# Kernel tuning notes

Measured on AMD Instinct MI355X. Metric: run time of the kernel, lower is better.

The kernel has to match this reference:

```python
import jax, jax.numpy as jnp
import numpy as np
import math


def setup_inputs() -> dict:
    key = jax.random.key(0)
    ks = jax.random.split(key, 8)
    B, S, dim = 4, 1024, 2048
    H, D = 16, 128          # n_heads = dim // core_dim
    T = 1024                # cached kv length
    w_scale = 1.0 / math.sqrt(dim)
    return {
        "x": jax.random.normal(ks[0], (B, S, dim), dtype=jnp.float32),
        "k_cache": jax.random.normal(ks[1], (B, H, T, D), dtype=jnp.float32),
        "v_cache": jax.random.normal(ks[2], (B, H, T, D), dtype=jnp.float32),
        "Wq": jax.random.normal(ks[3], (dim, dim), dtype=jnp.float32) * w_scale,
        "bq": jnp.zeros((dim,), jnp.float32),
        "Wk": jax.random.normal(ks[4], (dim, dim), dtype=jnp.float32) * w_scale,
        "bk": jnp.zeros((dim,), jnp.float32),
        "Wv": jax.random.normal(ks[5], (dim, dim), dtype=jnp.float32) * w_scale,
        "bv": jnp.zeros((dim,), jnp.float32),
        "Wo": jax.random.normal(ks[6], (dim, dim), dtype=jnp.float32) * w_scale,
        "bo": jnp.zeros((dim,), jnp.float32),
    }


def _split_heads(t, H):
    # [B, S, dim] -> [B, H, S, D]
    B, S, dim = t.shape
    return t.reshape(B, S, H, dim // H).transpose(0, 2, 1, 3)


def reference(x, k_cache, v_cache, Wq, bq, Wk, bk, Wv, bv, Wo, bo):
    B, S, dim = x.shape
    H = k_cache.shape[1]
    D = dim // H
    T = k_cache.shape[2]

    q = _split_heads(x @ Wq.T + bq, H)                 # [B,H,S,D]
    k_new = _split_heads(x @ Wk.T + bk, H)             # [B,H,S,D]
    v_new = _split_heads(x @ Wv.T + bv, H)

    k = jnp.concatenate([k_cache, k_new], axis=2)      # [B,H,T+S,D]
    v = jnp.concatenate([v_cache, v_new], axis=2)

    scale = 1.0 / math.sqrt(D)
    scores = jnp.einsum("bhqd,bhkd->bhqk", q, k) * scale   # [B,H,S,T+S]

    # causal mask with cache offset: query i may attend to key j iff j <= i + T
    q_pos = jnp.arange(S)[:, None] + T
    k_pos = jnp.arange(T + S)[None, :]
    mask = k_pos <= q_pos                              # [S, T+S]
    scores = jnp.where(mask[None, None], scores, jnp.finfo(scores.dtype).min)

    attn = jax.nn.softmax(scores, axis=-1)
    ctx = jnp.einsum("bhqk,bhkd->bhqd", attn, v)       # [B,H,S,D]
    ctx = ctx.transpose(0, 2, 1, 3).reshape(B, S, dim) # merge heads

    out = ctx @ Wo.T + bo                              # dropout is identity (p=0 / eval)
    return (out, k, v)
```

## Files before the change

kernel.cpp:

```cpp
#include <hip/hip_runtime.h>
#include <hip/hip_bf16.h>

typedef float f32x4 __attribute__((ext_vector_type(4)));
typedef __bf16 bf16x8 __attribute__((ext_vector_type(8)));
typedef unsigned short u16x8 __attribute__((ext_vector_type(8)));

#define DIMK 2048
#define QSCALE ((float)(0.08838834764831845 * 1.4426950408889634))

__device__ __forceinline__ unsigned short f2bf(float f) {
    union { float f; unsigned int u; } v; v.f = f;
    unsigned int r = v.u + 0x7fffu + ((v.u >> 16) & 1u);
    return (unsigned short)(r >> 16);
}
__device__ __forceinline__ float bf2f(unsigned short u) {
    union { unsigned int i; float f; } v; v.i = ((unsigned int)u) << 16; return v.f;
}

__device__ __forceinline__ void lds_load16(void* lds, const void* gsrc) {
    __builtin_amdgcn_global_load_lds(
        (const __attribute__((address_space(1))) unsigned int*)gsrc,
        (__attribute__((address_space(3))) unsigned int*)lds,
        16, 0, 0);
}

__device__ __forceinline__ int vperm4(int kv4) {
    return ((kv4 >> 5) << 5) + (((kv4 >> 2) & 3) << 3) + (((kv4 >> 4) & 1) << 2);
}

__global__ __launch_bounds__(256) void prep_all(
    const float* __restrict__ x,  const float* __restrict__ Wq,
    const float* __restrict__ Wk, const float* __restrict__ Wv,
    const float* __restrict__ Wo,
    const float* __restrict__ kc, const float* __restrict__ vc,
    unsigned short* __restrict__ xbf, unsigned short* __restrict__ Wqb,
    unsigned short* __restrict__ Wkb, unsigned short* __restrict__ Wvb,
    unsigned short* __restrict__ Wob,
    float* __restrict__ kout, unsigned short* __restrict__ Kbf,
    float* __restrict__ vout, unsigned short* __restrict__ Vtp)
{
    const int bid = blockIdx.x;
    const int tid = threadIdx.x;

    if (bid < 24576) {
        int i = bid * 256 + tid;
        const float* src; unsigned short* dst; size_t off;
        if (i < 2097152) { src = x; dst = xbf; off = i; }
        else {
            int j = (i - 2097152) >> 20;
            off = (size_t)((i - 2097152) & 1048575);
            src = j == 0 ? Wq : j == 1 ? Wk : j == 2 ? Wv : Wo;
            dst = j == 0 ? Wqb : j == 1 ? Wkb : j == 2 ? Wvb : Wob;
        }
        f32x4 v = *(const f32x4*)(src + off * 4);
        ushort4 pk = { f2bf(v[0]), f2bf(v[1]), f2bf(v[2]), f2bf(v[3]) };
        *(ushort4*)(dst + off * 4) = pk;
    } else if (bid < 32768) {
        size_t i4 = (size_t)(bid - 24576) * 256 + tid;
        size_t e = i4 * 4;
        size_t bh = e >> 17, rem = e & 131071;
        f32x4 v = *(const f32x4*)(kc + e);
        size_t dsto = (bh << 18) + rem;
        *(f32x4*)(kout + dsto) = v;
        ushort4 pk = { f2bf(v[0]), f2bf(v[1]), f2bf(v[2]), f2bf(v[3]) };
        *(ushort4*)(Kbf + dsto) = pk;
    } else {
        __shared__ unsigned short T[128 * 72];
        const int o = bid - 32768;
        const int t = o & 15;
        const int kv0 = t * 64;
        const int bh = o >> 4;
        const float* src = vc + ((size_t)bh << 17) + (size_t)kv0 * 128;
        float* vdst = vout + ((size_t)bh << 18) + (size_t)kv0 * 128;
        #pragma unroll
        for (int r = 0; r < 8; ++r) {
            int e4 = r * 256 + tid;
            int kv = e4 >> 5, d0 = (e4 & 31) << 2;
            f32x4 v = *(const f32x4*)(src + kv * 128 + d0);
            *(f32x4*)(vdst + kv * 128 + d0) = v;
            #pragma unroll
            for (int i = 0; i < 4; ++i) T[(d0 + i) * 72 + kv] = f2bf(v[i]);
        }
        __syncthreads();
        unsigned short* tile = Vtp + ((size_t)bh * 32 + t) * 8192;
        #pragma unroll
        for (int r = 0; r < 8; ++r) {
            int e = r * 256 + tid;
            int d = e >> 4, k4 = (e & 15) << 2;
            ushort4 pk = { T[d * 72 + k4], T[d * 72 + k4 + 1], T[d * 72 + k4 + 2], T[d * 72 + k4 + 3] };
            const int idx = d * 64 + (vperm4(k4) ^ ((d & 7) << 3));
            *(ushort4*)(tile + idx) = pk;
        }
    }
}

__device__ __forceinline__ void gemm_core64(
    const unsigned short* __restrict__ A16, const unsigned short* __restrict__ W16,
    int m0, int n0, int tid, int w, int g, int c, int wr, int wc,
    unsigned short* As, unsigned short* Bs, f32x4 (&acc)[4][4])
{
    const int srow = tid >> 3;
    const int schk = (tid & 7) ^ (srow & 7);
    const unsigned short* Asrc = A16 + (size_t)(m0 + srow) * DIMK + schk * 8;
    const unsigned short* Bsrc = W16 + (size_t)(n0 + srow) * DIMK + schk * 8;
    const int cswz = (c & 7) << 3;

    for (int k0 = 0; k0 < DIMK; k0 += 64) {
        __syncthreads();
        #pragma unroll
        for (int r = 0; r < 4; ++r) {
            lds_load16(As + r * 2048 + w * 512, Asrc + (size_t)r * 32 * DIMK + k0);
            lds_load16(Bs + r * 2048 + w * 512, Bsrc + (size_t)r * 32 * DIMK + k0);
        }
        __syncthreads();

        #pragma unroll
        for (int kd = 0; kd < 2; ++kd) {
            const int ko = (kd * 32 + g * 8) ^ cswz;
            bf16x8 af[4], bfr[4];
            #pragma unroll
            for (int i = 0; i < 4; ++i)
                af[i] = *(const bf16x8*)(&As[(wr * 64 + i * 16 + c) * 64 + ko]);
            #pragma unroll
            for (int i = 0; i < 4; ++i)
                bfr[i] = *(const bf16x8*)(&Bs[(wc * 64 + i * 16 + c) * 64 + ko]);
            #pragma unroll
            for (int i = 0; i < 4; ++i)
                #pragma unroll
                for (int j = 0; j < 4; ++j)
                    acc[i][j] = __builtin_amdgcn_mfma_f32_16x16x32_bf16(af[i], bfr[j], acc[i][j], 0, 0, 0);
        }
    }
}

__global__ __launch_bounds__(256) void gemm_qkv(
    const unsigned short* __restrict__ xbf,
    const unsigned short* __restrict__ Wqb, const unsigned short* __restrict__ Wkb,
    const unsigned short* __restrict__ Wvb,
    const float* __restrict__ bq, const float* __restrict__ bk, const float* __restrict__ bv,
    unsigned short* __restrict__ Qbf,
    float* __restrict__ kout, unsigned short* __restrict__ Kbf,
    float* __restrict__ vout, unsigned short* __restrict__ Vtp)
{
    const int o = blockIdx.x;
    const int xcd = o & 7;
    const int k = o >> 3;
    const int mblk = k & 31;
    const int nloc = k >> 5;
    const int nblk = xcd * 6 + nloc;
    const int m0 = mblk * 128;
    const int n0g = nblk * 128;
    const int mi = n0g >> 11;
    const int n0 = n0g & 2047;

    const unsigned short* W16 = mi == 0 ? Wqb : (mi == 1 ? Wkb : Wvb);
    const float* bias = mi == 0 ? bq : (mi == 1 ? bk : bv);

    const int tid = threadIdx.x;
    const int lane = tid & 63;
    const int w = tid >> 6;
    const int g = lane >> 4;
    const int c = lane & 15;
    const int wr = w >> 1, wc = w & 1;

    __shared__ unsigned short As[128 * 64];
    __shared__ unsigned short Bs[128 * 64];

    f32x4 acc[4][4];
    #pragma unroll
    for (int i = 0; i < 4; ++i)
        #pragma unroll
        for (int j = 0; j < 4; ++j)
            acc[i][j] = f32x4{0.f, 0.f, 0.f, 0.f};

    gemm_core64(xbf, W16, m0, n0, tid, w, g, c, wr, wc, As, Bs, acc);

    #pragma unroll
    for (int j = 0; j < 4; ++j) {
        const int n = n0 + wc * 64 + j * 16 + c;
        const float bn = bias[n];
        const int hh = n >> 7, d = n & 127;
        #pragma unroll
        for (int i = 0; i < 4; ++i) {
            float y4[4];
            #pragma unroll
            for (int tq = 0; tq < 4; ++tq) y4[tq] = acc[i][j][tq] + bn;
            const int mb = m0 + wr * 64 + i * 16 + g * 4;
            if (mi == 0) {
                #pragma unroll
                for (int tq = 0; tq < 4; ++tq) {
                    int m = mb + tq; int b = m >> 10, s = m & 1023;
                    Qbf[((((size_t)b * 16 + hh) << 10) + s) * 128 + d] = f2bf(y4[tq] * QSCALE);
                }
            } else if (mi == 1) {
                #pragma unroll
                for (int tq = 0; tq < 4; ++tq) {
                    int m = mb + tq; int b = m >> 10, s = m & 1023;
                    kout[(((size_t)b * 16 + hh) * 2048 + 1024 + s) * 128 + d] = y4[tq];
                    Kbf[(((size_t)b * 16 + hh) << 18) + (size_t)(1024 + s) * 128 + d] = f2bf(y4[tq]);
                }
            } else {
                #pragma unroll
                for (int tq = 0; tq < 4; ++tq) {
                    int m = mb + tq; int b = m >> 10, s = m & 1023;
                    vout[(((size_t)b * 16 + hh) * 2048 + 1024 + s) * 128 + d] = y4[tq];
                }
                int b = mb >> 10, s = mb & 1023;
                const int t = 16 + (s >> 6);
                const int idx = d * 64 + (vperm4(s & 63) ^ ((d & 7) << 3));
                ushort4 pk = { f2bf(y4[0]), f2bf(y4[1]), f2bf(y4[2]), f2bf(y4[3]) };
                *(ushort4*)(Vtp + ((size_t)(b * 16 + hh) * 32 + t) * 8192 + idx) = pk;
            }
        }
    }
}

__global__ __launch_bounds__(256) void gemm_wo(
    const unsigned short* __restrict__ ctx, const unsigned short* __restrict__ Wob,
    const float* __restrict__ bo, float* __restrict__ outp)
{
    const int o = blockIdx.x;
    const int xcd = o & 7;
    const int k = o >> 3;
    const int mblk = k & 31;
    const int nloc = k >> 5;
    const int nblk = xcd * 2 + nloc;
    const int m0 = mblk * 128;
    const int n0 = nblk * 128;

    const int tid = threadIdx.x;
    const int lane = tid & 63;
    const int w = tid >> 6;
    const int g = lane >> 4;
    const int c = lane & 15;
    const int wr = w >> 1, wc = w & 1;

    __shared__ unsigned short As[128 * 64];
    __shared__ unsigned short Bs[128 * 64];

    f32x4 acc[4][4];
    #pragma unroll
    for (int i = 0; i < 4; ++i)
        #pragma unroll
        for (int j = 0; j < 4; ++j)
            acc[i][j] = f32x4{0.f, 0.f, 0.f, 0.f};

    gemm_core64(ctx, Wob, m0, n0, tid, w, g, c, wr, wc, As, Bs, acc);

    #pragma unroll
    for (int j = 0; j < 4; ++j) {
        const int n = n0 + wc * 64 + j * 16 + c;
        const float bn = bo[n];
        #pragma unroll
        for (int i = 0; i < 4; ++i) {
            const int mb = m0 + wr * 64 + i * 16 + g * 4;
            #pragma unroll
            for (int tq = 0; tq < 4; ++tq)
                outp[(size_t)(mb + tq) * 2048 + n] = acc[i][j][tq] + bn;
        }
    }
}

__global__ __launch_bounds__(512) void attn9(
    const unsigned short* __restrict__ Qbf,
    const unsigned short* __restrict__ Kbf,
    const unsigned short* __restrict__ Vtp,
    unsigned short* __restrict__ Pp,
    float* __restrict__ Mp,
    float* __restrict__ Lp)
{
    const int o = blockIdx.x;
    const int xcd = o & 7;
    const int kk0 = o >> 3;
    const int half = kk0 & 1;
    const int qt = 7 - ((kk0 >> 1) & 7);
    const int bh = (kk0 >> 4) * 8 + xcd;

    const int tid = threadIdx.x;
    const int lane = tid & 63;
    const int w = tid >> 6;
    const int g = lane >> 4;
    const int c = lane & 15;
    const int cswz = (c & 7) << 3;

    __shared__ unsigned short Ks[2][64 * 128];
    __shared__ unsigned short Vs[2][64 * 128];

    const unsigned short* Qb = Qbf + ((size_t)bh * 1024 + qt * 128) * 128;
    const unsigned short* Kb = Kbf + ((size_t)bh << 18);
    const unsigned short* Vtile = Vtp + (size_t)bh * 32 * 8192;

    bf16x8 aq[4];
    #pragma unroll
    for (int kd = 0; kd < 4; ++kd)
        aq[kd] = *(const bf16x8*)(Qb + (w * 16 + c) * 128 + kd * 32 + g * 8);

    f32x4 od[8];
    #pragma unroll
    for (int nf = 0; nf < 8; ++nf)
        od[nf] = f32x4{0.f, 0.f, 0.f, 0.f};
    float mrow = -1e30f, lrow = 0.f;

    const int krow = tid >> 4;
    const int kswz = (((tid & 15) << 4) ^ ((krow & 7) << 4)) >> 1;
    const unsigned short* Kl = Kb + (size_t)krow * 128 + kswz;

    const int cnt = 9 + qt;
    const int t0 = half * cnt;
    const int limw = 1024 + qt * 128 + w * 16;

    {
        const int kv0 = t0 * 64;
        lds_load16(&Ks[0][w * 512], Kl + (size_t)kv0 * 128);
        lds_load16(&Ks[0][4096 + w * 512], Kl + (size_t)(kv0 + 32) * 128);
        const unsigned short* Vsrc = Vtile + (size_t)t0 * 8192 + tid * 8;
        lds_load16(&Vs[0][w * 512], Vsrc);
        lds_load16(&Vs[0][4096 + w * 512], Vsrc + 4096);
        __syncthreads();
    }

    int cur = 0;
    for (int t = t0; t < t0 + cnt; ++t) {
        const int kv0 = t * 64;
        const bool next = (t + 1 < t0 + cnt);

        if (next) {
            const int kvn = kv0 + 64;
            lds_load16(&Ks[cur ^ 1][w * 512], Kl + (size_t)kvn * 128);
            lds_load16(&Ks[cur ^ 1][4096 + w * 512], Kl + (size_t)(kvn + 32) * 128);
            const unsigned short* Vsrc = Vtile + (size_t)(t + 1) * 8192 + tid * 8;
            lds_load16(&Vs[cur ^ 1][w * 512], Vsrc);
            lds_load16(&Vs[cur ^ 1][4096 + w * 512], Vsrc + 4096);
        }

        const unsigned short* Ksc = &Ks[cur][0];
        const unsigned short* Vsc = &Vs[cur][0];

        f32x4 sc[4];
        #pragma unroll
        for (int n = 0; n < 4; ++n)
            sc[n] = f32x4{0.f, 0.f, 0.f, 0.f};
        #pragma unroll
        for (int kd = 0; kd < 4; ++kd) {
            bf16x8 bk[4];
            #pragma unroll
            for (int n = 0; n < 4; ++n)
                bk[n] = *(const bf16x8*)(&Ksc[(n * 16 + c) * 128 + ((kd * 32 + g * 8) ^ cswz)]);
            #pragma unroll
            for (int n = 0; n < 4; ++n)
                sc[n] = __builtin_amdgcn_mfma_f32_16x16x32_bf16(bk[n], aq[kd], sc[n], 0, 0, 0);
        }

        const bool need_mask = (kv0 + 63 > limw);
        if (need_mask) {
            const int lim = limw + c;
            #pragma unroll
            for (int n = 0; n < 4; ++n)
                #pragma unroll
                for (int j = 0; j < 4; ++j)
                    if (kv0 + n * 16 + g * 4 + j > lim) sc[n][j] = -1e30f;
        }
        {
            float t4[4];
            #pragma unroll
            for (int n = 0; n < 4; ++n)
                t4[n] = fmaxf(fmaxf(sc[n][0], sc[n][1]), fmaxf(sc[n][2], sc[n][3]));
            float rmax = fmaxf(fmaxf(t4[0], t4[1]), fmaxf(t4[2], t4[3]));
            rmax = fmaxf(rmax, __shfl_xor(rmax, 16));
            rmax = fmaxf(rmax, __shfl_xor(rmax, 32));

            if (!__all(rmax <= mrow + 8.0f)) {
                const float mnew = fmaxf(mrow, rmax);
                const float fs = exp2f(mrow - mnew);
                mrow = mnew;
                lrow *= fs;
                #pragma unroll
                for (int j = 0; j < 4; ++j) {
                    const float fsj = __shfl(fs, (lane & 48) | (g * 4 + j));
                    #pragma unroll
                    for (int nf = 0; nf < 8; ++nf)
                        od[nf][j] *= fsj;
                }
            }
            const float mm = mrow;
            float s4[4];
            #pragma unroll
            for (int n = 0; n < 4; ++n) {
                #pragma unroll
                for (int j = 0; j < 4; ++j)
                    sc[n][j] = exp2f(sc[n][j] - mm);
                s4[n] = (sc[n][0] + sc[n][1]) + (sc[n][2] + sc[n][3]);
            }
            float rsum = (s4[0] + s4[1]) + (s4[2] + s4[3]);
            rsum += __shfl_xor(rsum, 16);
            rsum += __shfl_xor(rsum, 32);
            lrow += rsum;
        }

        bf16x8 pa[2];
        #pragma unroll
        for (int kk = 0; kk < 2; ++kk)
            #pragma unroll
            for (int e = 0; e < 8; ++e)
                pa[kk][e] = (__bf16)sc[2 * kk + (e >> 2)][e & 3];

        #pragma unroll
        for (int kk = 0; kk < 2; ++kk) {
            #pragma unroll
            for (int nf = 0; nf < 8; ++nf) {
                bf16x8 bv = *(const bf16x8*)(&Vsc[(nf * 16 + c) * 64 + ((kk * 32 + g * 8) ^ cswz)]);
                od[nf] = __builtin_amdgcn_mfma_f32_16x16x32_bf16(pa[kk], bv, od[nf], 0, 0, 0);
            }
        }

        __syncthreads();
        cur ^= 1;
    }

    const size_t pbase = ((size_t)(half * 64 + bh) * 1024 + qt * 128) * 128;
    const int mlbase = (half * 64 + bh) * 1024 + qt * 128;
    if (lane < 16) {
        Mp[mlbase + w * 16 + c] = mrow;
        Lp[mlbase + w * 16 + c] = lrow;
    }
    #pragma unroll
    for (int j = 0; j < 4; ++j) {
        const float lj = __shfl(lrow, (lane & 48) | (g * 4 + j));
        const float rl = 1.0f / lj;
        const int ql = w * 16 + g * 4 + j;
        #pragma unroll
        for (int nf = 0; nf < 8; ++nf)
            Pp[pbase + (size_t)ql * 128 + nf * 16 + c] = f2bf(od[nf][j] * rl);
    }
}

__global__ __launch_bounds__(256) void merge_ctx(
    const unsigned short* __restrict__ Pp, const float* __restrict__ Mp,
    const float* __restrict__ Lp, unsigned short* __restrict__ ctx)
{
    const int idx = blockIdx.x * 256 + threadIdx.x;
    const int r = idx >> 4;
    const int dc = (idx & 15) << 3;
    const float m0 = Mp[r], m1 = Mp[65536 + r];
    const float l0 = Lp[r], l1 = Lp[65536 + r];
    const float M = fmaxf(m0, m1);
    float w0 = l0 * exp2f(m0 - M);
    float w1 = l1 * exp2f(m1 - M);
    const float inv = 1.0f / (w0 + w1);
    w0 *= inv; w1 *= inv;
    u16x8 a = *(const u16x8*)(Pp + (size_t)r * 128 + dc);
    u16x8 bb = *(const u16x8*)(Pp + (size_t)8388608 + (size_t)r * 128 + dc);
    const int bh = r >> 10, q = r & 1023;
    unsigned short* dst = ctx + ((size_t)(bh >> 4) * 1024 + q) * 2048 + (bh & 15) * 128 + dc;
    u16x8 outv;
    #pragma unroll
    for (int e = 0; e < 8; ++e)
        outv[e] = f2bf(w0 * bf2f(a[e]) + w1 * bf2f(bb[e]));
    *(u16x8*)dst = outv;
}

__global__ __launch_bounds__(256) void copy_cache(
    const float* __restrict__ kc, const float* __restrict__ vc,
    float* __restrict__ kout, float* __restrict__ vout)
{
    size_t i4 = (size_t)blockIdx.x * 256 + threadIdx.x;
    const float* src = blockIdx.y ? vc : kc;
    float* dst = blockIdx.y ? vout : kout;
    size_t e = i4 * 4;
    size_t bh = e >> 17, rem = e & 131071;
    f32x4 v = *(const f32x4*)(src + e);
    *(f32x4*)(dst + (bh << 18) + rem) = v;
}

template<int MODE, bool ABF16>
__global__ __launch_bounds__(256) void gemm_bt(
    const void* __restrict__ Ag, const float* __restrict__ Wf,
    const float* __restrict__ bias, void* __restrict__ dst)
{
    const int tid = threadIdx.x;
    const int lane = tid & 63;
    const int w = tid >> 6;
    const int g = lane >> 4;
    const int c = lane & 15;
    const int wr = w >> 1, wc = w & 1;
    const int m0 = blockIdx.y * 128;
    const int n0 = blockIdx.x * 128;

    __shared__ unsigned short As[128 * 40];
    __shared__ unsigned short Bs[128 * 40];

    f32x4 acc[4][4];
    #pragma unroll
    for (int i = 0; i < 4; ++i)
        #pragma unroll
        for (int j = 0; j < 4; ++j)
            acc[i][j] = f32x4{0.f, 0.f, 0.f, 0.f};

    for (int k0 = 0; k0 < DIMK; k0 += 32) {
        __syncthreads();
        if constexpr (ABF16) {
            const unsigned short* A16 = (const unsigned short*)Ag;
            #pragma unroll
            for (int r = 0; r < 2; ++r) {
                int e8 = r * 256 + tid;
                int row = e8 >> 2, col = (e8 & 3) << 3;
                *(uint4*)(&As[row * 40 + col]) =
                    *(const uint4*)(A16 + (size_t)(m0 + row) * DIMK + k0 + col);
            }
        } else {
            const float* Af = (const float*)Ag;
            #pragma unroll
            for (int r = 0; r < 4; ++r) {
                int e4 = r * 256 + tid;
                int row = e4 >> 3, col = (e4 & 7) << 2;
                f32x4 v = *(const f32x4*)(Af + (size_t)(m0 + row) * DIMK + k0 + col);
                ushort4 pk = { f2bf(v[0]), f2bf(v[1]), f2bf(v[2]), f2bf(v[3]) };
                *(ushort4*)(&As[row * 40 + col]) = pk;
            }
        }
        {
            #pragma unroll
            for (int r = 0; r < 4; ++r) {
                int e4 = r * 256 + tid;
                int row = e4 >> 3, col = (e4 & 7) << 2;
                f32x4 v = *(const f32x4*)(Wf + (size_t)(n0 + row) * DIMK + k0 + col);
                ushort4 pk = { f2bf(v[0]), f2bf(v[1]), f2bf(v[2]), f2bf(v[3]) };
                *(ushort4*)(&Bs[row * 40 + col]) = pk;
            }
        }
        __syncthreads();

        bf16x8 af[4], bfr[4];
        #pragma unroll
        for (int i = 0; i < 4; ++i)
            af[i] = *(const bf16x8*)(&As[(wr * 64 + i * 16 + c) * 40 + g * 8]);
        #pragma unroll
        for (int i = 0; i < 4; ++i)
            bfr[i] = *(const bf16x8*)(&Bs[(wc * 64 + i * 16 + c) * 40 + g * 8]);
        #pragma unroll
        for (int i = 0; i < 4; ++i)
            #pragma unroll
            for (int j = 0; j < 4; ++j)
                acc[i][j] = __builtin_amdgcn_mfma_f32_16x16x32_bf16(af[i], bfr[j], acc[i][j], 0, 0, 0);
    }

    #pragma unroll
    for (int j = 0; j < 4; ++j) {
        const int n = n0 + wc * 64 + j * 16 + c;
        const float bn = bias[n];
        #pragma unroll
        for (int i = 0; i < 4; ++i) {
            float y4[4];
            #pragma unroll
            for (int tq = 0; tq < 4; ++tq) y4[tq] = acc[i][j][tq] + bn;
            const int mb = m0 + wr * 64 + i * 16 + g * 4;
            if constexpr (MODE == 0) {
                #pragma unroll
                for (int tq = 0; tq < 4; ++tq) {
                    int m = mb + tq; int b = m >> 10, s = m & 1023;
                    int hh = n >> 7, d = n & 127;
                    ((unsigned short*)dst)[((((size_t)b * 16 + hh) << 10) + s) * 128 + d] = f2bf(y4[tq] * QSCALE);
                }
            } else if constexpr (MODE == 1) {
                #pragma unroll
                for (int tq = 0; tq < 4; ++tq) {
                    int m = mb + tq; int b = m >> 10, s = m & 1023;
                    int hh = n >> 7, d = n & 127;
                    ((float*)dst)[(((size_t)b * 16 + hh) * 2048 + 1024 + s) * 128 + d] = y4[tq];
                }
            } else {
                #pragma unroll
                for (int tq = 0; tq < 4; ++tq)
                    ((float*)dst)[(size_t)(mb + tq) * 2048 + n] = y4[tq];
            }
        }
    }
}

__global__ __launch_bounds__(256) void attn_stage(
    const unsigned short* __restrict__ Qbf,
    const float* __restrict__ Kf, const float* __restrict__ Vf,
    unsigned short* __restrict__ ctx)
{
    const int qt = blockIdx.x;
    const int bh = blockIdx.y;
    const int b = bh >> 4, h = bh & 15;
    const int tid = threadIdx.x;
    const int lane = tid & 63;
    const int w = tid >> 6;
    const int g = lane >> 4;
    const int c = lane & 15;

    __shared__ unsigned short Ksl[64 * 136];
    __shared__ unsigned short Vtl[128 * 72];
    __shared__ unsigned short Ps[4 * 32 * 72];

    bf16x8 aq[2][4];
    const unsigned short* Qb = Qbf + ((size_t)bh * 1024 + qt * 128) * 128;
    #pragma unroll
    for (int m2 = 0; m2 < 2; ++m2)
        #pragma unroll
        for (int kk = 0; kk < 4; ++kk)
            aq[m2][kk] = *(const bf16x8*)(Qb + (w * 32 + m2 * 16 + c) * 128 + kk * 32 + g * 8);

    f32x4 od[2][8];
    #pragma unroll
    for (int m2 = 0; m2 < 2; ++m2)
        #pragma unroll
        for (int nf = 0; nf < 8; ++nf)
            od[m2][nf] = f32x4{0.f, 0.f, 0.f, 0.f};
    float mrow[2][4], lrow[2][4];
    #pragma unroll
    for (int m2 = 0; m2 < 2; ++m2)
        #pragma unroll
        for (int j = 0; j < 4; ++j) { mrow[m2][j] = -1e30f; lrow[m2][j] = 0.f; }

    const float* Kb = Kf + (size_t)bh * 2048 * 128;
    const float* Vb = Vf + (size_t)bh * 2048 * 128;
    const int ntiles = 18 + 2 * qt;

    for (int t = 0; t < ntiles; ++t) {
        __syncthreads();
        const float* Kt = Kb + (size_t)t * 64 * 128;
        #pragma unroll
        for (int r = 0; r < 8; ++r) {
            int e4 = r * 256 + tid;
            int kv = e4 >> 5, d0 = (e4 & 31) << 2;
            f32x4 v = *(const f32x4*)(Kt + kv * 128 + d0);
            ushort4 pk = { f2bf(v[0]), f2bf(v[1]), f2bf(v[2]), f2bf(v[3]) };
            *(ushort4*)(&Ksl[kv * 136 + d0]) = pk;
        }
        const float* Vg = Vb + (size_t)t * 64 * 128;
        #pragma unroll
        for (int r = 0; r < 8; ++r) {
            int e4 = tid * 8 + r;
            int kv = e4 >> 5, d0 = (e4 & 31) << 2;
            f32x4 v = *(const f32x4*)(Vg + kv * 128 + d0);
            #pragma unroll
            for (int i = 0; i < 4; ++i)
                Vtl[(d0 + i) * 72 + kv] = f2bf(v[i]);
        }
        __syncthreads();

        f32x4 sc[2][4];
        #pragma unroll
        for (int m2 = 0; m2 < 2; ++m2)
            #pragma unroll
            for (int n = 0; n < 4; ++n)
                sc[m2][n] = f32x4{0.f, 0.f, 0.f, 0.f};
        #pragma unroll
        for (int kk = 0; kk < 4; ++kk) {
            bf16x8 bk[4];
            #pragma unroll
            for (int n = 0; n < 4; ++n)
                bk[n] = *(const bf16x8*)(&Ksl[(n * 16 + c) * 136 + kk * 32 + g * 8]);
            #pragma unroll
            for (int m2 = 0; m2 < 2; ++m2)
                #pragma unroll
                for (int n = 0; n < 4; ++n)
                    sc[m2][n] = __builtin_amdgcn_mfma_f32_16x16x32_bf16(aq[m2][kk], bk[n], sc[m2][n], 0, 0, 0);
        }

        const int kvbase = t * 64;
        #pragma unroll
        for (int m2 = 0; m2 < 2; ++m2) {
            #pragma unroll
            for (int j = 0; j < 4; ++j) {
                const int qg = qt * 128 + w * 32 + m2 * 16 + g * 4 + j;
                const int lim = qg + 1024;
                float rmax = -1e30f;
                #pragma unroll
                for (int n = 0; n < 4; ++n) {
                    float s = sc[m2][n][j] * QSCALE;
                    if (kvbase + n * 16 + c > lim) s = -1e30f;
                    sc[m2][n][j] = s;
                    rmax = fmaxf(rmax, s);
                }
                #pragma unroll
                for (int off = 1; off < 16; off <<= 1)
                    rmax = fmaxf(rmax, __shfl_xor(rmax, off));
                float mold = mrow[m2][j];
                float mnew = fmaxf(mold, rmax);
                mrow[m2][j] = mnew;
                float fs = exp2f(mold - mnew);
                float rsum = 0.f;
                #pragma unroll
                for (int n = 0; n < 4; ++n) {
                    float p = exp2f(sc[m2][n][j] - mnew);
                    sc[m2][n][j] = p;
                    rsum += p;
                }
                #pragma unroll
                for (int off = 1; off < 16; off <<= 1)
                    rsum += __shfl_xor(rsum, off);
                lrow[m2][j] = lrow[m2][j] * fs + rsum;
                #pragma unroll
                for (int nf = 0; nf < 8; ++nf)
                    od[m2][nf][j] *= fs;
            }
        }

        unsigned short* Pw = &Ps[w * 32 * 72];
        #pragma unroll
        for (int m2 = 0; m2 < 2; ++m2)
            #pragma unroll
            for (int n = 0; n < 4; ++n)
                #pragma unroll
                for (int j = 0; j < 4; ++j)
                    Pw[(m2 * 16 + g * 4 + j) * 72 + n * 16 + c] = f2bf(sc[m2][n][j]);

        #pragma unroll
        for (int kk = 0; kk < 2; ++kk) {
            bf16x8 ap0 = *(const bf16x8*)(&Ps[(w * 32 + c) * 72 + kk * 32 + g * 8]);
            bf16x8 ap1 = *(const bf16x8*)(&Ps[(w * 32 + 16 + c) * 72 + kk * 32 + g * 8]);
            #pragma unroll
            for (int nf = 0; nf < 8; ++nf) {
                bf16x8 bv = *(const bf16x8*)(&Vtl[(nf * 16 + c) * 72 + kk * 32 + g * 8]);
                od[0][nf] = __builtin_amdgcn_mfma_f32_16x16x32_bf16(ap0, bv, od[0][nf], 0, 0, 0);
                od[1][nf] = __builtin_amdgcn_mfma_f32_16x16x32_bf16(ap1, bv, od[1][nf], 0, 0, 0);
            }
        }
    }

    #pragma unroll
    for (int m2 = 0; m2 < 2; ++m2) {
        #pragma unroll
        for (int j = 0; j < 4; ++j) {
            const int qg = qt * 128 + w * 32 + m2 * 16 + g * 4 + j;
            const float rl = 1.0f / lrow[m2][j];
            #pragma unroll
            for (int nf = 0; nf < 8; ++nf) {
                const int d = nf * 16 + c;
                ctx[((size_t)b * 1024 + qg) * 2048 + h * 128 + d] = f2bf(od[m2][nf][j] * rl);
            }
        }
    }
}

extern "C" void kernel_launch(void* const* d_in, const int* in_sizes, int n_in,
                              void* d_out, int out_size, void* d_ws, size_t ws_size,
                              hipStream_t stream) {
    const float* x  = (const float*)d_in[0];
    const float* kc = (const float*)d_in[1];
    const float* vc = (const float*)d_in[2];
    const float* Wq = (const float*)d_in[3];
    const float* bq = (const float*)d_in[4];
    const float* Wk = (const float*)d_in[5];
    const float* bk = (const float*)d_in[6];
    const float* Wv = (const float*)d_in[7];
    const float* bv = (const float*)d_in[8];
    const float* Wo = (const float*)d_in[9];
    const float* bo = (const float*)d_in[10];

    float* outp = (float*)d_out;
    float* kout = outp + (size_t)8388608;
    float* vout = outp + (size_t)25165824;

    unsigned short* Qbf = (unsigned short*)d_ws;
    unsigned short* ctx = Qbf + (size_t)8388608;
    unsigned short* Kbf = ctx + (size_t)8388608;
    unsigned short* Vtp = Kbf + (size_t)16777216;
    unsigned short* xbf = Vtp + (size_t)16777216;
    unsigned short* Wqb = xbf + (size_t)8388608;
    unsigned short* Wkb = Wqb + (size_t)4194304;
    unsigned short* Wvb = Wkb + (size_t)4194304;
    unsigned short* Wob = Wvb + (size_t)4194304;
    unsigned short* Pp = xbf;
    float* Mp = (float*)Wvb;
    float* Lp = Mp + (size_t)131072;

    const bool full = ws_size >= (size_t)150994944;

    if (full) {
        prep_all<<<33792, 256, 0, stream>>>(x, Wq, Wk, Wv, Wo, kc, vc,
                                            xbf, Wqb, Wkb, Wvb, Wob,
                                            kout, Kbf, vout, Vtp);
        gemm_qkv<<<1536, 256, 0, stream>>>(xbf, Wqb, Wkb, Wvb, bq, bk, bv,
                                           Qbf, kout, Kbf, vout, Vtp);
        attn9<<<1024, 512, 0, stream>>>(Qbf, Kbf, Vtp, Pp, Mp, Lp);
        merge_ctx<<<4096, 256, 0, stream>>>(Pp, Mp, Lp, ctx);
        gemm_wo<<<512, 256, 0, stream>>>(ctx, Wob, bo, outp);
    } else {
        copy_cache<<<dim3(8192, 2), 256, 0, stream>>>(kc, vc, kout, vout);
        gemm_bt<0, false><<<dim3(16, 32), 256, 0, stream>>>(x, Wq, bq, Qbf);
        gemm_bt<1, false><<<dim3(16, 32), 256, 0, stream>>>(x, Wk, bk, kout);
        gemm_bt<1, false><<<dim3(16, 32), 256, 0, stream>>>(x, Wv, bv, vout);
        attn_stage<<<dim3(8, 64), 256, 0, stream>>>(Qbf, kout, vout, ctx);
        gemm_bt<2, true><<<dim3(16, 32), 256, 0, stream>>>(ctx, Wo, bo, outp);
    }
}
```

Measured before the change: 367.7 us.

## Double-buffer LDS tiles in projection GEMM core to overlap loads with MFMA

The shared GEMM core used by the QKV and output projections now uses two LDS buffers per operand. The next K-tile is loaded asynchronously into the alternate buffer while MFMAs run on the current one, with one barrier per iteration instead of two. This aims to hide global-to-LDS latency, at the cost of doubled LDS use (64KB per block), which may reduce occupancy. The global_load_lds writes rely on the single barrier for completion ordering, with no explicit vmcnt wait visible.

```diff
diff --git a/kernel.cpp b/kernel.cpp
--- a/kernel.cpp
+++ b/kernel.cpp
@@ -94,7 +94,7 @@
     }
 }
 
-__device__ __forceinline__ void gemm_core64(
+__device__ __forceinline__ void gemm_core64db(
     const unsigned short* __restrict__ A16, const unsigned short* __restrict__ W16,
     int m0, int n0, int tid, int w, int g, int c, int wr, int wc,
     unsigned short* As, unsigned short* Bs, f32x4 (&acc)[4][4])
@@ -105,14 +105,29 @@
     const unsigned short* Bsrc = W16 + (size_t)(n0 + srow) * DIMK + schk * 8;
     const int cswz = (c & 7) << 3;
 
-    for (int k0 = 0; k0 < DIMK; k0 += 64) {
-        __syncthreads();
-        #pragma unroll
-        for (int r = 0; r < 4; ++r) {
-            lds_load16(As + r * 2048 + w * 512, Asrc + (size_t)r * 32 * DIMK + k0);
-            lds_load16(Bs + r * 2048 + w * 512, Bsrc + (size_t)r * 32 * DIMK + k0);
-        }
-        __syncthreads();
+    #pragma unroll
+    for (int r = 0; r < 4; ++r) {
+        lds_load16(As + r * 2048 + w * 512, Asrc + (size_t)r * 32 * DIMK);
+        lds_load16(Bs + r * 2048 + w * 512, Bsrc + (size_t)r * 32 * DIMK);
+    }
+    __syncthreads();
+
+    #pragma unroll 2
+    for (int t = 0; t < 32; ++t) {
+        const int cur = t & 1;
+        const unsigned short* Ac = As + cur * 8192;
+        const unsigned short* Bc = Bs + cur * 8192;
+
+        if (t + 1 < 32) {
+            unsigned short* An = As + (cur ^ 1) * 8192;
+            unsigned short* Bn = Bs + (cur ^ 1) * 8192;
+            const int k0 = (t + 1) * 64;
+            #pragma unroll
+            for (int r = 0; r < 4; ++r) {
+                lds_load16(An + r * 2048 + w * 512, Asrc + (size_t)r * 32 * DIMK + k0);
+                lds_load16(Bn + r * 2048 + w * 512, Bsrc + (size_t)r * 32 * DIMK + k0);
+            }
+        }
 
         #pragma unroll
         for (int kd = 0; kd < 2; ++kd) {
@@ -120,16 +135,18 @@
             bf16x8 af[4], bfr[4];
             #pragma unroll
             for (int i = 0; i < 4; ++i)
-                af[i] = *(const bf16x8*)(&As[(wr * 64 + i * 16 + c) * 64 + ko]);
+                af[i] = *(const bf16x8*)(&Ac[(wr * 64 + i * 16 + c) * 64 + ko]);
             #pragma unroll
             for (int i = 0; i < 4; ++i)
-                bfr[i] = *(const bf16x8*)(&Bs[(wc * 64 + i * 16 + c) * 64 + ko]);
+                bfr[i] = *(const bf16x8*)(&Bc[(wc * 64 + i * 16 + c) * 64 + ko]);
             #pragma unroll
             for (int i = 0; i < 4; ++i)
                 #pragma unroll
                 for (int j = 0; j < 4; ++j)
                     acc[i][j] = __builtin_amdgcn_mfma_f32_16x16x32_bf16(af[i], bfr[j], acc[i][j], 0, 0, 0);
         }
+
+        __syncthreads();
     }
 }
 
@@ -163,8 +180,8 @@
     const int c = lane & 15;
     const int wr = w >> 1, wc = w & 1;
 
-    __shared__ unsigned short As[128 * 64];
-    __shared__ unsigned short Bs[128 * 64];
+    __shared__ unsigned short As[2 * 128 * 64];
+    __shared__ unsigned short Bs[2 * 128 * 64];
 
     f32x4 acc[4][4];
     #pragma unroll
@@ -173,7 +190,7 @@
         for (int j = 0; j < 4; ++j)
             acc[i][j] = f32x4{0.f, 0.f, 0.f, 0.f};
 
-    gemm_core64(xbf, W16, m0, n0, tid, w, g, c, wr, wc, As, Bs, acc);
+    gemm_core64db(xbf, W16, m0, n0, tid, w, g, c, wr, wc, As, Bs, acc);
 
     #pragma unroll
     for (int j = 0; j < 4; ++j) {
@@ -235,8 +252,8 @@
     const int c = lane & 15;
     const int wr = w >> 1, wc = w & 1;
 
-    __shared__ unsigned short As[128 * 64];
-    __shared__ unsigned short Bs[128 * 64];
+    __shared__ unsigned short As[2 * 128 * 64];
+    __shared__ unsigned short Bs[2 * 128 * 64];
 
     f32x4 acc[4][4];
     #pragma unroll
@@ -245,7 +262,7 @@
         for (int j = 0; j < 4; ++j)
             acc[i][j] = f32x4{0.f, 0.f, 0.f, 0.f};
 
-    gemm_core64(ctx, Wob, m0, n0, tid, w, g, c, wr, wc, As, Bs, acc);
+    gemm_core64db(ctx, Wob, m0, n0, tid, w, g, c, wr, wc, As, Bs, acc);
 
     #pragma unroll
     for (int j = 0; j < 4; ++j) {
```

Result: slower. 404.3 us (+10.0%).
